# Optimization experiments

Measured on AMD Instinct MI355X. Metric: run time of the kernel, lower is better.

## Reference

```python
import jax, jax.numpy as jnp
import numpy as np

B, T, D, H = 4, 2048, 768, 12
HD = D // H  # head size 64
DF = 3072    # feed-forward size


def setup_inputs() -> dict:
    key = jax.random.key(0)
    ks = jax.random.split(key, 10)
    s = 0.02
    return {
        "x": jax.random.normal(ks[0], (B, T, D), jnp.float32),
        "mask": jnp.ones((B, T), jnp.int32),
        "Wq": jax.random.normal(ks[1], (D, D), jnp.float32) * s,
        "bq": jnp.zeros((D,), jnp.float32),
        "Wk": jax.random.normal(ks[2], (D, D), jnp.float32) * s,
        "bk": jnp.zeros((D,), jnp.float32),
        "Wv": jax.random.normal(ks[3], (D, D), jnp.float32) * s,
        "bv": jnp.zeros((D,), jnp.float32),
        "Wo": jax.random.normal(ks[4], (D, D), jnp.float32) * s,
        "bo": jnp.zeros((D,), jnp.float32),
        "W1": jax.random.normal(ks[5], (D, DF), jnp.float32) * s,
        "b1": jnp.zeros((DF,), jnp.float32),
        "W2": jax.random.normal(ks[6], (DF, D), jnp.float32) * s,
        "b2": jnp.zeros((D,), jnp.float32),
    }


def reference(x, mask, Wq, bq, Wk, bk, Wv, bv, Wo, bo, W1, b1, W2, b2):
    scale = 1.0 / np.sqrt(HD).astype(np.float32)
    # projections -> [B, H, T, HD]
    def split_heads(t):
        return t.reshape(B, T, H, HD).transpose(0, 2, 1, 3)
    q = split_heads(x @ Wq + bq)
    k = split_heads(x @ Wk + bk)
    v = split_heads(x @ Wv + bv)
    # [B, H, T, T] attention scores (materialized, as in the original)
    scores = jnp.einsum('bhqd,bhkd->bhqk', q, k) * scale
    neg_inf = jnp.float32(-jnp.inf)
    scores = jnp.where(mask[:, None, None, :] == 0, neg_inf, scores)
    attn = jax.nn.softmax(scores, axis=-1)
    ctx = jnp.einsum('bhqk,bhkd->bhqd', attn, v)          # [B,H,T,HD]
    ctx = ctx.transpose(0, 2, 1, 3).reshape(B, T, D)       # merge heads
    attn_out = ctx @ Wo + bo
    h = x + attn_out                                       # residual 1 (dropout p=0)
    ff = jax.nn.gelu(h @ W1 + b1, approximate=False) @ W2 + b2
    out = h + ff                                           # residual 2
    return out, attn
```

## Files before the change

### kernel.cpp

```cpp
#include <hip/hip_runtime.h>
#include <hip/hip_bf16.h>
#include <math.h>

typedef unsigned short u16;
typedef __attribute__((ext_vector_type(8))) short short8;
typedef __attribute__((ext_vector_type(4))) float f32x4;

constexpr int Bc = 4, Tt = 2048, Dd = 768, Hh = 12, Hd = 64, Df = 3072;
constexpr int BT = Bc * Tt;

__device__ __forceinline__ u16 f2b(float x) {
  __hip_bfloat16 h = __float2bfloat16(x);
  return *reinterpret_cast<u16*>(&h);
}
__device__ __forceinline__ float b2f(u16 v) {
  unsigned int u = ((unsigned int)v) << 16;
  return __builtin_bit_cast(float, u);
}
__device__ __forceinline__ float gelu_exact(float g) {
  return 0.5f * g * (1.0f + erff(g * 0.70710678118654752440f));
}
__device__ __forceinline__ void gload16(const void* g, void* l) {
  __builtin_amdgcn_global_load_lds(
      (const __attribute__((address_space(1))) unsigned int*)g,
      (__attribute__((address_space(3))) unsigned int*)l, 16, 0, 0);
}

__device__ __forceinline__ void tr_tile(const float* __restrict__ in,
                                        u16* __restrict__ out, int R, int C,
                                        int bx, int by, float* sh) {
  const int tx = threadIdx.x & 31, ty = threadIdx.x >> 5;
  const int r0 = by * 32, c0 = bx * 32;
#pragma unroll
  for (int i = 0; i < 4; ++i)
    sh[(ty + i * 8) * 33 + tx] = in[(size_t)(r0 + ty + i * 8) * C + c0 + tx];
  __syncthreads();
#pragma unroll
  for (int i = 0; i < 4; ++i)
    out[(size_t)(c0 + ty + i * 8) * R + r0 + tx] = f2b(sh[tx * 33 + ty + i * 8]);
}

__global__ __launch_bounds__(256) void prep_all(
    const float* __restrict__ x, const float* __restrict__ Wq,
    const float* __restrict__ Wk, const float* __restrict__ Wv,
    const float* __restrict__ Wo, const float* __restrict__ W1,
    const float* __restrict__ W2, const float* __restrict__ bq,
    const float* __restrict__ bk, const float* __restrict__ bv,
    const int* __restrict__ mask, u16* __restrict__ xb,
    u16* __restrict__ wqkvT, u16* __restrict__ woT, u16* __restrict__ w1T,
    u16* __restrict__ w2T, float* __restrict__ biasc,
    unsigned int* __restrict__ mwords) {
  __shared__ float sh[32 * 33];
  const int s = blockIdx.x;
  if (s < 3072) {
    int i = (s * 256 + threadIdx.x) * 8;
    float4 a = *(const float4*)&x[i];
    float4 b = *(const float4*)&x[i + 4];
    u16 t[8] = {f2b(a.x), f2b(a.y), f2b(a.z), f2b(a.w),
                f2b(b.x), f2b(b.y), f2b(b.z), f2b(b.w)};
    *(uint4*)&xb[i] = *(uint4*)t;
  } else if (s < 3648) {
    int u = s - 3072; tr_tile(Wq, wqkvT, Dd, Dd, u % 24, u / 24, sh);
  } else if (s < 4224) {
    int u = s - 3648; tr_tile(Wk, wqkvT + 768 * Dd, Dd, Dd, u % 24, u / 24, sh);
  } else if (s < 4800) {
    int u = s - 4224; tr_tile(Wv, wqkvT + 1536 * Dd, Dd, Dd, u % 24, u / 24, sh);
  } else if (s < 5376) {
    int u = s - 4800; tr_tile(Wo, woT, Dd, Dd, u % 24, u / 24, sh);
  } else if (s < 7680) {
    int u = s - 5376; tr_tile(W1, w1T, Dd, Df, u % 96, u / 96, sh);
  } else if (s < 9984) {
    int u = s - 7680; tr_tile(W2, w2T, Df, Dd, u % 24, u / 24, sh);
  } else if (s < 9993) {
    int i = (s - 9984) * 256 + threadIdx.x;
    biasc[i] = (i < 768) ? bq[i] : (i < 1536) ? bk[i - 768] : bv[i - 1536];
  } else {
    const int id = threadIdx.x;
    const int b_ = id >> 6, kv0 = (id & 63) * 32;
    unsigned int wbits = 0u;
    for (int j = 0; j < 32; ++j)
      wbits |= (mask[b_ * Tt + kv0 + j] ? 1u : 0u) << j;
    mwords[id] = wbits;
  }
}

template <int MODE>
__global__ __launch_bounds__(256) void mgemm(
    const u16* __restrict__ A, const u16* __restrict__ Bt,
    const float* __restrict__ bias, const float* __restrict__ add,
    const u16* __restrict__ addb, void* __restrict__ C0,
    void* __restrict__ C1, void* __restrict__ C2, int K, int N) {
  __shared__ __align__(16) u16 As[2][128 * 32];
  __shared__ __align__(16) u16 Bs[2][128 * 32];
  const int tid = threadIdx.x;
  const int lane = tid & 63, wv = tid >> 6;
  const int m0 = blockIdx.y * 128, n0 = blockIdx.x * 128;
  const int wm = (wv >> 1) * 64, wn = (wv & 1) * 64;

  f32x4 acc[4][4] = {};

#define MG_STAGE(k0_, bf_)                                                    \
  {                                                                           \
    _Pragma("unroll") for (int i_ = 0; i_ < 2; ++i_) {                        \
      const int idx_ = i_ * 256 + tid;                                        \
      const int row_ = idx_ >> 2;                                             \
      const int kc_ = (idx_ & 3) * 8;                                         \
      const u16* ga_;                                                         \
      if constexpr (MODE == 2) {                                              \
        const int m_ = m0 + row_, b_ = m_ >> 11, t_ = m_ & 2047;              \
        const int kk_ = (k0_) + kc_, hd_ = kk_ >> 6, d_ = kk_ & 63;           \
        ga_ = &A[(((size_t)(b_ * Hh + hd_) * Tt + t_) << 6) + d_];            \
      } else {                                                                \
        ga_ = &A[(size_t)(m0 + row_) * K + (k0_) + kc_];                      \
      }                                                                       \
      gload16(ga_, &As[bf_][idx_ * 8]);                                       \
      gload16(&Bt[(size_t)(n0 + row_) * K + (k0_) + kc_], &Bs[bf_][idx_ * 8]);\
    }                                                                         \
  }

  MG_STAGE(0, 0);
  __syncthreads();

  int it = 0;
  for (int k0 = 0; k0 < K; k0 += 32, ++it) {
    const int cur = it & 1;
    if (k0 + 32 < K) MG_STAGE(k0 + 32, cur ^ 1);
    short8 af[4], bfr[4];
#pragma unroll
    for (int i = 0; i < 4; ++i) {
      af[i] = *reinterpret_cast<const short8*>(
          &As[cur][(wm + i * 16 + (lane & 15)) * 32 + (lane >> 4) * 8]);
      bfr[i] = *reinterpret_cast<const short8*>(
          &Bs[cur][(wn + i * 16 + (lane & 15)) * 32 + (lane >> 4) * 8]);
    }
#pragma unroll
    for (int i = 0; i < 4; ++i)
#pragma unroll
      for (int j = 0; j < 4; ++j)
        acc[i][j] = __builtin_amdgcn_mfma_f32_16x16x32_bf16(af[i], bfr[j],
                                                            acc[i][j], 0, 0, 0);
    __syncthreads();
  }
#undef MG_STAGE

  const int lr = (lane >> 4) * 4, lc = lane & 15;
#pragma unroll
  for (int i = 0; i < 4; ++i) {
    const int mbase = m0 + wm + i * 16 + lr;
#pragma unroll
    for (int j = 0; j < 4; ++j) {
      const int col = n0 + wn + j * 16 + lc;
      const float bvs = bias[col];
#pragma unroll
      for (int r = 0; r < 4; ++r) {
        const int m = mbase + r;
        float g = acc[i][j][r] + bvs;
        if constexpr (MODE == 5) {
          const int b = m >> 11, t = m & 2047;
          if (col < 768) {
            const int head = col >> 6, d = col & 63;
            ((u16*)C0)[(((size_t)(b * Hh + head) * Tt + t) << 6) + d] = f2b(g);
          } else if (col < 1536) {
            const int c = col - 768, head = c >> 6, d = c & 63;
            ((u16*)C1)[(((size_t)(b * Hh + head) * Tt + t) << 6) + d] = f2b(g);
          } else {
            const int c = col - 1536, head = c >> 6, d = c & 63;
            ((u16*)C2)[(((size_t)(b * Hh + head) * Hd + d) << 11) + t] = f2b(g);
          }
        } else if constexpr (MODE == 2) {
          g += add[(size_t)m * Dd + col];
          ((u16*)C0)[(size_t)m * Dd + col] = f2b(g);
        } else if constexpr (MODE == 3) {
          ((u16*)C0)[(size_t)m * N + col] = f2b(gelu_exact(g));
        } else {
          g += b2f(addb[(size_t)m * Dd + col]);
          ((float*)C0)[(size_t)m * Dd + col] = g;
        }
      }
    }
  }
}

__global__ __launch_bounds__(256) void attn_fused(
    const u16* __restrict__ qb, const u16* __restrict__ kb,
    const u16* __restrict__ vtb, const unsigned int* __restrict__ mwords,
    float* __restrict__ attn, u16* __restrict__ ctxb) {
  const int bh = blockIdx.y;
  const int b = bh / Hh;
  const int q0 = blockIdx.x * 64;
  const u16* Qg = qb + (size_t)bh * Tt * Hd;
  const u16* Kg = kb + (size_t)bh * Tt * Hd;
  const u16* Vg = vtb + (size_t)bh * Hd * Tt;
  float* attng = attn + (size_t)bh * Tt * Tt;
  u16* ctxg = ctxb + (size_t)bh * Tt * Hd;
  const unsigned int* mwp = mwords + b * 64;

  __shared__ __align__(16) u16 Ks[2][128 * 64];
  __shared__ __align__(16) u16 Vs[2][64 * 128];
  __shared__ __align__(16) u16 Ps[64 * 128];

  const int tid = threadIdx.x, lane = tid & 63, wv = tid >> 6;
  const int lc = lane & 15, lg = lane >> 4;
  const int ql = wv * 16 + lc;
  const int qsw = lc & 7;

#define STAGE_K(t, bf)                                                       \
  {                                                                          \
    const int kv0_ = (t) * 128;                                              \
    _Pragma("unroll") for (int w_ = 0; w_ < 4; ++w_) {                       \
      const int p_ = w_ * 256 + tid;                                         \
      const int row_ = p_ >> 3, kc8_ = (p_ & 7) ^ (row_ & 7);                \
      gload16(Kg + (size_t)(kv0_ + row_) * Hd + kc8_ * 8, &Ks[bf][p_ * 8]);  \
    }                                                                        \
  }
#define STAGE_V(t, bf)                                                       \
  {                                                                          \
    const int kv0_ = (t) * 128;                                              \
    _Pragma("unroll") for (int w_ = 0; w_ < 4; ++w_) {                       \
      const int p_ = w_ * 256 + tid;                                         \
      const int d_ = p_ >> 4, pc_ = (p_ & 15) ^ (d_ & 7);                    \
      gload16(Vg + (size_t)d_ * Tt + kv0_ + pc_ * 8, &Vs[bf][p_ * 8]);       \
    }                                                                        \
  }
#define FENCE() asm volatile("" ::: "memory")

  short8 qf[2];
#pragma unroll
  for (int ks = 0; ks < 2; ++ks)
    qf[ks] = *(const short8*)&Qg[(size_t)(q0 + ql) * Hd + ks * 32 + lg * 8];

  float l = 0.f;

  STAGE_K(0, 0);
  for (int t = 0; t < 16; ++t) {
    asm volatile("s_waitcnt vmcnt(0)" ::: "memory");
    __builtin_amdgcn_s_barrier();
    FENCE();
    const int bf = t & 1;
    if (t < 15) STAGE_K(t + 1, bf ^ 1);
    f32x4 s[8] = {};
#pragma unroll
    for (int ks = 0; ks < 2; ++ks) {
      const int ph = (ks * 4 + lg) ^ qsw;
#pragma unroll
      for (int i = 0; i < 8; ++i) {
        const short8 af = *(const short8*)&Ks[bf][(i * 16 + lc) * 64 + ph * 8];
        s[i] = __builtin_amdgcn_mfma_f32_16x16x32_bf16(af, qf[ks], s[i], 0, 0, 0);
      }
    }
    const uint4 mw4 = *(const uint4*)&mwp[t * 4];
    const unsigned int mwa[4] = {mw4.x, mw4.y, mw4.z, mw4.w};
    float ts = 0.f;
#pragma unroll
    for (int i = 0; i < 8; ++i) {
      const unsigned int w = mwa[i >> 1];
#pragma unroll
      for (int r = 0; r < 4; ++r) {
        const float bit = (float)((w >> ((i & 1) * 16 + lg * 4 + r)) & 1u);
        ts += __expf(s[i][r] * 0.125f) * bit;
      }
    }
    ts += __shfl_xor(ts, 16);
    ts += __shfl_xor(ts, 32);
    l += ts;
  }

  const float linv = 1.f / l;
  f32x4 cacc[4] = {};

  __builtin_amdgcn_s_barrier();
  FENCE();

  STAGE_K(0, 0);
  STAGE_V(0, 0);
  for (int t = 0; t < 16; ++t) {
    const int kv0 = t * 128;
    const int bf = t & 1;
    if (t == 0)
      asm volatile("s_waitcnt vmcnt(0)" ::: "memory");
    else
      asm volatile("s_waitcnt vmcnt(8)" ::: "memory");
    __builtin_amdgcn_s_barrier();
    FENCE();
    if (t < 15) {
      STAGE_K(t + 1, bf ^ 1);
      STAGE_V(t + 1, bf ^ 1);
    }
    f32x4 s[8] = {};
#pragma unroll
    for (int ks = 0; ks < 2; ++ks) {
      const int ph = (ks * 4 + lg) ^ qsw;
#pragma unroll
      for (int i = 0; i < 8; ++i) {
        const short8 af = *(const short8*)&Ks[bf][(i * 16 + lc) * 64 + ph * 8];
        s[i] = __builtin_amdgcn_mfma_f32_16x16x32_bf16(af, qf[ks], s[i], 0, 0, 0);
      }
    }
    const uint4 mw4 = *(const uint4*)&mwp[t * 4];
    const unsigned int mwa[4] = {mw4.x, mw4.y, mw4.z, mw4.w};
#pragma unroll
    for (int i = 0; i < 8; ++i) {
      const unsigned int w = mwa[i >> 1];
      u16 pb[4];
#pragma unroll
      for (int r = 0; r < 4; ++r) {
        const float bit = (float)((w >> ((i & 1) * 16 + lg * 4 + r)) & 1u);
        pb[r] = f2b(__expf(s[i][r] * 0.125f) * bit * linv);
      }
      const int chunk = i * 2 + (lg >> 1);
      const int ph2 = chunk ^ qsw;
      *(uint2*)&Ps[ql * 128 + ph2 * 8 + (lg & 1) * 4] = *(uint2*)pb;
    }
#pragma unroll
    for (int ks = 0; ks < 4; ++ks) {
      const short8 pa =
          *(const short8*)&Ps[ql * 128 + ((ks * 4 + lg) ^ qsw) * 8];
#pragma unroll
      for (int j2 = 0; j2 < 4; ++j2) {
        const int d = j2 * 16 + lc;
        const short8 vb2 =
            *(const short8*)&Vs[bf][d * 128 + (((ks * 4 + lg) ^ (d & 7))) * 8];
        cacc[j2] =
            __builtin_amdgcn_mfma_f32_16x16x32_bf16(pa, vb2, cacc[j2], 0, 0, 0);
      }
    }
#pragma unroll
    for (int it2 = 0; it2 < 8; ++it2) {
      const int row = wv * 16 + it2 * 2 + (lane >> 5);
      const int colg = lane & 31;
      const int chunk = colg >> 1, half = colg & 1;
      const uint2 pr = *(const uint2*)&Ps[row * 128 +
                                          (chunk ^ (row & 7)) * 8 + half * 4];
      f32x4 v;
      v[0] = b2f((u16)(pr.x & 0xffffu));
      v[1] = b2f((u16)(pr.x >> 16));
      v[2] = b2f((u16)(pr.y & 0xffffu));
      v[3] = b2f((u16)(pr.y >> 16));
      __builtin_nontemporal_store(
          v, (f32x4*)&attng[(size_t)(q0 + row) * Tt + kv0 + colg * 4]);
    }
  }

#pragma unroll
  for (int j2 = 0; j2 < 4; ++j2)
#pragma unroll
    for (int r = 0; r < 4; ++r) {
      const int q = q0 + wv * 16 + lg * 4 + r;
      ctxg[(size_t)q * Hd + j2 * 16 + lc] = f2b(cacc[j2][r]);
    }
#undef STAGE_K
#undef STAGE_V
#undef FENCE
}

extern "C" void kernel_launch(void* const* d_in, const int* in_sizes, int n_in,
                              void* d_out, int out_size, void* d_ws,
                              size_t ws_size, hipStream_t stream) {
  const float* x = (const float*)d_in[0];
  const int* mask = (const int*)d_in[1];
  const float* Wq = (const float*)d_in[2];
  const float* bq = (const float*)d_in[3];
  const float* Wk = (const float*)d_in[4];
  const float* bk = (const float*)d_in[5];
  const float* Wv = (const float*)d_in[6];
  const float* bv = (const float*)d_in[7];
  const float* Wo = (const float*)d_in[8];
  const float* bo = (const float*)d_in[9];
  const float* W1 = (const float*)d_in[10];
  const float* b1 = (const float*)d_in[11];
  const float* W2 = (const float*)d_in[12];
  const float* b2 = (const float*)d_in[13];

  float* out = (float*)d_out;
  float* attn = out + (size_t)BT * Dd;

  char* w = (char*)d_ws;
  u16* xb = (u16*)w;      w += (size_t)BT * Dd * 2;
  u16* wqkvT = (u16*)w;   w += (size_t)Dd * 2304 * 2;
  u16* woT = (u16*)w;     w += (size_t)Dd * Dd * 2;
  u16* w1T = (u16*)w;     w += (size_t)Dd * Df * 2;
  u16* w2T = (u16*)w;     w += (size_t)Df * Dd * 2;
  float* biasc = (float*)w;            w += 2304 * 4;
  unsigned int* mwords = (unsigned int*)w; w += 256 * 4;
  u16* qb = (u16*)w;      w += (size_t)BT * Dd * 2;
  u16* kb = (u16*)w;      w += (size_t)BT * Dd * 2;
  u16* vtb = (u16*)w;     w += (size_t)BT * Dd * 2;
  u16* ctxb = (u16*)w;    w += (size_t)BT * Dd * 2;
  u16* ff1b = (u16*)w;    w += (size_t)BT * Df * 2;
  u16* hb = vtb;

  dim3 blk(256);

  prep_all<<<dim3(9994), blk, 0, stream>>>(x, Wq, Wk, Wv, Wo, W1, W2, bq, bk,
                                           bv, mask, xb, wqkvT, woT, w1T, w2T,
                                           biasc, mwords);

  mgemm<5><<<dim3(18, 64), blk, 0, stream>>>(xb, wqkvT, biasc, nullptr, nullptr,
                                             qb, kb, vtb, Dd, 2304);

  attn_fused<<<dim3(32, 48), blk, 0, stream>>>(qb, kb, vtb, mwords, attn, ctxb);

  mgemm<2><<<dim3(6, 64), blk, 0, stream>>>(ctxb, woT, bo, x, nullptr, hb,
                                            nullptr, nullptr, Dd, Dd);

  mgemm<3><<<dim3(24, 64), blk, 0, stream>>>(hb, w1T, b1, nullptr, nullptr,
                                             ff1b, nullptr, nullptr, Dd, Df);

  mgemm<4><<<dim3(6, 64), blk, 0, stream>>>(ff1b, w2T, b2, nullptr, hb, out,
                                            nullptr, nullptr, Df, Dd);
}
```

Baseline: 474.5 us.

## Split attention-weight write into separate pass co-scheduled with FF1 GEMM

The attention kernel no longer writes the 805MB fp32 attention matrix. It now only computes the context and stores each row's inverse softmax denominator to workspace. A new combined kernel interleaves FF1 GEMM tiles (odd blocks) with blocks that recompute QK^T and write normalized attention weights (even blocks). The goal is to overlap the memory-bound attn store with compute-bound FF1 work. The cost is recomputing the score MFMAs, and the ctx loop now waits with vmcnt(0) instead of vmcnt(8), which drops the prefetch overlap.

```diff
diff --git a/kernel.cpp b/kernel.cpp
--- a/kernel.cpp
+++ b/kernel.cpp
@@ -25,6 +25,7 @@
       (const __attribute__((address_space(1))) unsigned int*)g,
       (__attribute__((address_space(3))) unsigned int*)l, 16, 0, 0);
 }
+#define FENCE() asm volatile("" ::: "memory")
 
 __device__ __forceinline__ void tr_tile(const float* __restrict__ in,
                                         u16* __restrict__ out, int R, int C,
@@ -170,8 +171,6 @@
         } else if constexpr (MODE == 2) {
           g += add[(size_t)m * Dd + col];
           ((u16*)C0)[(size_t)m * Dd + col] = f2b(g);
-        } else if constexpr (MODE == 3) {
-          ((u16*)C0)[(size_t)m * N + col] = f2b(gelu_exact(g));
         } else {
           g += b2f(addb[(size_t)m * Dd + col]);
           ((float*)C0)[(size_t)m * Dd + col] = g;
@@ -181,17 +180,16 @@
   }
 }
 
-__global__ __launch_bounds__(256) void attn_fused(
+__global__ __launch_bounds__(256) void attn_ctx(
     const u16* __restrict__ qb, const u16* __restrict__ kb,
     const u16* __restrict__ vtb, const unsigned int* __restrict__ mwords,
-    float* __restrict__ attn, u16* __restrict__ ctxb) {
+    float* __restrict__ linv_ws, u16* __restrict__ ctxb) {
   const int bh = blockIdx.y;
   const int b = bh / Hh;
   const int q0 = blockIdx.x * 64;
   const u16* Qg = qb + (size_t)bh * Tt * Hd;
   const u16* Kg = kb + (size_t)bh * Tt * Hd;
   const u16* Vg = vtb + (size_t)bh * Hd * Tt;
-  float* attng = attn + (size_t)bh * Tt * Tt;
   u16* ctxg = ctxb + (size_t)bh * Tt * Hd;
   const unsigned int* mwp = mwords + b * 64;
 
@@ -222,7 +220,6 @@
       gload16(Vg + (size_t)d_ * Tt + kv0_ + pc_ * 8, &Vs[bf][p_ * 8]);       \
     }                                                                        \
   }
-#define FENCE() asm volatile("" ::: "memory")
 
   short8 qf[2];
 #pragma unroll
@@ -266,6 +263,7 @@
   }
 
   const float linv = 1.f / l;
+  if (lg == 0) linv_ws[(size_t)bh * Tt + q0 + ql] = linv;
   f32x4 cacc[4] = {};
 
   __builtin_amdgcn_s_barrier();
@@ -274,12 +272,8 @@
   STAGE_K(0, 0);
   STAGE_V(0, 0);
   for (int t = 0; t < 16; ++t) {
-    const int kv0 = t * 128;
     const int bf = t & 1;
-    if (t == 0)
-      asm volatile("s_waitcnt vmcnt(0)" ::: "memory");
-    else
-      asm volatile("s_waitcnt vmcnt(8)" ::: "memory");
+    asm volatile("s_waitcnt vmcnt(0)" ::: "memory");
     __builtin_amdgcn_s_barrier();
     FENCE();
     if (t < 15) {
@@ -324,21 +318,6 @@
             __builtin_amdgcn_mfma_f32_16x16x32_bf16(pa, vb2, cacc[j2], 0, 0, 0);
       }
     }
-#pragma unroll
-    for (int it2 = 0; it2 < 8; ++it2) {
-      const int row = wv * 16 + it2 * 2 + (lane >> 5);
-      const int colg = lane & 31;
-      const int chunk = colg >> 1, half = colg & 1;
-      const uint2 pr = *(const uint2*)&Ps[row * 128 +
-                                          (chunk ^ (row & 7)) * 8 + half * 4];
-      f32x4 v;
-      v[0] = b2f((u16)(pr.x & 0xffffu));
-      v[1] = b2f((u16)(pr.x >> 16));
-      v[2] = b2f((u16)(pr.y & 0xffffu));
-      v[3] = b2f((u16)(pr.y >> 16));
-      __builtin_nontemporal_store(
-          v, (f32x4*)&attng[(size_t)(q0 + row) * Tt + kv0 + colg * 4]);
-    }
   }
 
 #pragma unroll
@@ -350,7 +329,162 @@
     }
 #undef STAGE_K
 #undef STAGE_V
-#undef FENCE
+}
+
+__global__ __launch_bounds__(256) void ff1_attnw(
+    const u16* __restrict__ hb, const u16* __restrict__ w1T,
+    const float* __restrict__ b1, u16* __restrict__ ff1b,
+    const u16* __restrict__ qb, const u16* __restrict__ kb,
+    const unsigned int* __restrict__ mwords,
+    const float* __restrict__ linv_ws, float* __restrict__ attn) {
+  __shared__ __align__(16) u16 smem[24576];
+  const int tid = threadIdx.x, lane = tid & 63, wv = tid >> 6;
+  const int u = blockIdx.x >> 1;
+
+  if (blockIdx.x & 1) {
+    const int m0 = (u / 24) * 128, n0 = (u % 24) * 128;
+    const int wm = (wv >> 1) * 64, wn = (wv & 1) * 64;
+    const int K = Dd;
+    f32x4 acc[4][4] = {};
+
+#define F1_STAGE(k0_, bf_)                                                    \
+    {                                                                         \
+      _Pragma("unroll") for (int i_ = 0; i_ < 2; ++i_) {                      \
+        const int idx_ = i_ * 256 + tid;                                      \
+        const int row_ = idx_ >> 2;                                           \
+        const int kc_ = (idx_ & 3) * 8;                                       \
+        gload16(&hb[(size_t)(m0 + row_) * K + (k0_) + kc_],                   \
+                &smem[(bf_) * 4096 + idx_ * 8]);                              \
+        gload16(&w1T[(size_t)(n0 + row_) * K + (k0_) + kc_],                  \
+                &smem[8192 + (bf_) * 4096 + idx_ * 8]);                       \
+      }                                                                       \
+    }
+    F1_STAGE(0, 0);
+    __syncthreads();
+    int it = 0;
+    for (int k0 = 0; k0 < K; k0 += 32, ++it) {
+      const int cur = it & 1;
+      if (k0 + 32 < K) F1_STAGE(k0 + 32, cur ^ 1);
+      short8 af[4], bfr[4];
+#pragma unroll
+      for (int i = 0; i < 4; ++i) {
+        af[i] = *reinterpret_cast<const short8*>(
+            &smem[cur * 4096 + (wm + i * 16 + (lane & 15)) * 32 +
+                  (lane >> 4) * 8]);
+        bfr[i] = *reinterpret_cast<const short8*>(
+            &smem[8192 + cur * 4096 + (wn + i * 16 + (lane & 15)) * 32 +
+                  (lane >> 4) * 8]);
+      }
+#pragma unroll
+      for (int i = 0; i < 4; ++i)
+#pragma unroll
+        for (int j = 0; j < 4; ++j)
+          acc[i][j] = __builtin_amdgcn_mfma_f32_16x16x32_bf16(
+              af[i], bfr[j], acc[i][j], 0, 0, 0);
+      __syncthreads();
+    }
+#undef F1_STAGE
+    const int lr = (lane >> 4) * 4, lc = lane & 15;
+#pragma unroll
+    for (int i = 0; i < 4; ++i) {
+      const int mbase = m0 + wm + i * 16 + lr;
+#pragma unroll
+      for (int j = 0; j < 4; ++j) {
+        const int col = n0 + wn + j * 16 + lc;
+        const float bvs = b1[col];
+#pragma unroll
+        for (int r = 0; r < 4; ++r)
+          ff1b[(size_t)(mbase + r) * Df + col] =
+              f2b(gelu_exact(acc[i][j][r] + bvs));
+      }
+    }
+  } else {
+    const int bh = u >> 5;
+    const int q0 = (u & 31) * 64;
+    const int b = bh / Hh;
+    const u16* Qg = qb + (size_t)bh * Tt * Hd;
+    const u16* Kg = kb + (size_t)bh * Tt * Hd;
+    float* attng = attn + (size_t)bh * Tt * Tt;
+    const unsigned int* mwp = mwords + b * 64;
+    const int lc = lane & 15, lg = lane >> 4;
+    const int ql = wv * 16 + lc;
+    const int qsw = lc & 7;
+
+#define AW_STAGE_K(t, bf)                                                     \
+    {                                                                         \
+      const int kv0_ = (t) * 128;                                             \
+      _Pragma("unroll") for (int w_ = 0; w_ < 4; ++w_) {                      \
+        const int p_ = w_ * 256 + tid;                                        \
+        const int row_ = p_ >> 3, kc8_ = (p_ & 7) ^ (row_ & 7);               \
+        gload16(Kg + (size_t)(kv0_ + row_) * Hd + kc8_ * 8,                   \
+                &smem[(bf) * 8192 + p_ * 8]);                                 \
+      }                                                                       \
+    }
+
+    short8 qf[2];
+#pragma unroll
+    for (int ks = 0; ks < 2; ++ks)
+      qf[ks] = *(const short8*)&Qg[(size_t)(q0 + ql) * Hd + ks * 32 + lg * 8];
+    const float linv = linv_ws[(size_t)bh * Tt + q0 + ql];
+
+    AW_STAGE_K(0, 0);
+    for (int t = 0; t < 16; ++t) {
+      const int kv0 = t * 128;
+      const int bf = t & 1;
+      if (t == 0)
+        asm volatile("s_waitcnt vmcnt(0)" ::: "memory");
+      else
+        asm volatile("s_waitcnt vmcnt(8)" ::: "memory");
+      __builtin_amdgcn_s_barrier();
+      FENCE();
+      if (t < 15) AW_STAGE_K(t + 1, bf ^ 1);
+      f32x4 s[8] = {};
+#pragma unroll
+      for (int ks = 0; ks < 2; ++ks) {
+        const int ph = (ks * 4 + lg) ^ qsw;
+#pragma unroll
+        for (int i = 0; i < 8; ++i) {
+          const short8 af = *(const short8*)&smem[bf * 8192 +
+                                                  (i * 16 + lc) * 64 + ph * 8];
+          s[i] = __builtin_amdgcn_mfma_f32_16x16x32_bf16(af, qf[ks], s[i], 0,
+                                                         0, 0);
+        }
+      }
+      const uint4 mw4 = *(const uint4*)&mwp[t * 4];
+      const unsigned int mwa[4] = {mw4.x, mw4.y, mw4.z, mw4.w};
+#pragma unroll
+      for (int i = 0; i < 8; ++i) {
+        const unsigned int w = mwa[i >> 1];
+        u16 pb[4];
+#pragma unroll
+        for (int r = 0; r < 4; ++r) {
+          const float bit = (float)((w >> ((i & 1) * 16 + lg * 4 + r)) & 1u);
+          pb[r] = f2b(__expf(s[i][r] * 0.125f) * bit * linv);
+        }
+        const int chunk = i * 2 + (lg >> 1);
+        const int ph2 = chunk ^ qsw;
+        *(uint2*)&smem[16384 + ql * 128 + ph2 * 8 + (lg & 1) * 4] =
+            *(uint2*)pb;
+      }
+#pragma unroll
+      for (int it2 = 0; it2 < 8; ++it2) {
+        const int row = wv * 16 + it2 * 2 + (lane >> 5);
+        const int colg = lane & 31;
+        const int chunk = colg >> 1, half = colg & 1;
+        const uint2 pr = *(const uint2*)&smem[16384 + row * 128 +
+                                              (chunk ^ (row & 7)) * 8 +
+                                              half * 4];
+        f32x4 v;
+        v[0] = b2f((u16)(pr.x & 0xffffu));
+        v[1] = b2f((u16)(pr.x >> 16));
+        v[2] = b2f((u16)(pr.y & 0xffffu));
+        v[3] = b2f((u16)(pr.y >> 16));
+        __builtin_nontemporal_store(
+            v, (f32x4*)&attng[(size_t)(q0 + row) * Tt + kv0 + colg * 4]);
+      }
+    }
+#undef AW_STAGE_K
+  }
 }
 
 extern "C" void kernel_launch(void* const* d_in, const int* in_sizes, int n_in,
@@ -382,6 +516,7 @@
   u16* w2T = (u16*)w;     w += (size_t)Df * Dd * 2;
   float* biasc = (float*)w;            w += 2304 * 4;
   unsigned int* mwords = (unsigned int*)w; w += 256 * 4;
+  float* linv_ws = (float*)w;          w += (size_t)48 * Tt * 4;
   u16* qb = (u16*)w;      w += (size_t)BT * Dd * 2;
   u16* kb = (u16*)w;      w += (size_t)BT * Dd * 2;
   u16* vtb = (u16*)w;     w += (size_t)BT * Dd * 2;
@@ -398,13 +533,14 @@
   mgemm<5><<<dim3(18, 64), blk, 0, stream>>>(xb, wqkvT, biasc, nullptr, nullptr,
                                              qb, kb, vtb, Dd, 2304);
 
-  attn_fused<<<dim3(32, 48), blk, 0, stream>>>(qb, kb, vtb, mwords, attn, ctxb);
+  attn_ctx<<<dim3(32, 48), blk, 0, stream>>>(qb, kb, vtb, mwords, linv_ws,
+                                             ctxb);
 
   mgemm<2><<<dim3(6, 64), blk, 0, stream>>>(ctxb, woT, bo, x, nullptr, hb,
                                             nullptr, nullptr, Dd, Dd);
 
-  mgemm<3><<<dim3(24, 64), blk, 0, stream>>>(hb, w1T, b1, nullptr, nullptr,
-                                             ff1b, nullptr, nullptr, Dd, Df);
+  ff1_attnw<<<dim3(3072), blk, 0, stream>>>(hb, w1T, b1, ff1b, qb, kb, mwords,
+                                            linv_ws, attn);
 
   mgemm<4><<<dim3(6, 64), blk, 0, stream>>>(ff1b, w2T, b2, nullptr, hb, out,
                                             nullptr, nullptr, Df, Dd);
```

After: 547.1 us. 15.3% more time.
